# Kernel optimization log

Measured on AMD Instinct MI355X. Metric: run time of the kernel, lower is better.

Reference implementation:

```python
import jax, jax.numpy as jnp
import numpy as np

N = 100000       # nodes
E = 1600000      # edges (before self loops)
F_IN = 128       # input features
H = 4            # heads
C1, C2 = 32, 16  # per-head channels of conv1/conv2


def setup_inputs() -> dict:
    key = jax.random.key(0)
    ks = jax.random.split(key, 12)
    x = jax.random.normal(ks[0], (N, F_IN), jnp.float32)
    edge_index = jax.random.randint(ks[1], (2, E), 0, N, dtype=jnp.int32)
    s1 = 1.0 / np.sqrt(F_IN)
    s2 = 1.0 / np.sqrt(H * C1)
    return {
        "x": x,
        "edge_index": edge_index,
        "W1": jax.random.normal(ks[2], (F_IN, H * C1), jnp.float32) * s1,
        "a_src1": jax.random.normal(ks[3], (1, H, C1), jnp.float32) * s1,
        "a_dst1": jax.random.normal(ks[4], (1, H, C1), jnp.float32) * s1,
        "b1": jnp.zeros((H * C1,), jnp.float32),
        "W2": jax.random.normal(ks[5], (H * C1, H * C2), jnp.float32) * s2,
        "a_src2": jax.random.normal(ks[6], (1, H, C2), jnp.float32) * s2,
        "a_dst2": jax.random.normal(ks[7], (1, H, C2), jnp.float32) * s2,
        "b2": jnp.zeros((H * C2,), jnp.float32),
        "fc_w": jax.random.normal(ks[8], (H * C2, 2), jnp.float32) * (1.0 / np.sqrt(H * C2)),
        "fc_b": jnp.zeros((2,), jnp.float32),
    }


def gat_layer(x, edge_index, W, a_src, a_dst, b, heads, ch):
    """PyG GATConv: concat=True, negative_slope=0.2 (self loops already in edge_index)."""
    n = x.shape[0]
    h = (x @ W).reshape(n, heads, ch)                      # [N,H,C]
    alpha_src = jnp.sum(h * a_src, axis=-1)                # [N,H]
    alpha_dst = jnp.sum(h * a_dst, axis=-1)                # [N,H]
    src, dst = edge_index[0], edge_index[1]                # edge j->i: src=j, dst=i
    e = jax.nn.leaky_relu(alpha_src[src] + alpha_dst[dst], 0.2)  # [E,H]
    # scatter-softmax over incoming edges of each destination node
    m = jax.ops.segment_max(e, dst, num_segments=n)
    m = jnp.where(jnp.isfinite(m), m, 0.0)
    ex = jnp.exp(e - m[dst])
    s = jax.ops.segment_sum(ex, dst, num_segments=n)
    alpha = ex / s[dst]                                    # self loops guarantee s > 0
    out = jax.ops.segment_sum(alpha[:, :, None] * h[src], dst, num_segments=n)
    return out.reshape(n, heads * ch) + b


def reference(x, edge_index, W1, a_src1, a_dst1, b1, W2, a_src2, a_dst2, b2, fc_w, fc_b):
    n = x.shape[0]
    loops = jnp.arange(n, dtype=edge_index.dtype)
    ei = jnp.concatenate([edge_index, jnp.stack([loops, loops])], axis=1)  # add self loops once
    h = jax.nn.relu(gat_layer(x, ei, W1, a_src1, a_dst1, b1, H, C1))
    h = gat_layer(h, ei, W2, a_src2, a_dst2, b2, H, C2)
    g = jnp.sum(h, axis=0, keepdims=True)  # global_add_pool, batch = all zeros -> single graph
    return g @ fc_w + fc_b
```

## Files before the change

### kernel.cpp

```cpp
#include <hip/hip_runtime.h>
#include <hip/hip_bf16.h>
#include <math.h>


__device__ __forceinline__ float b2f(unsigned short u) {
    return __uint_as_float(((unsigned)u) << 16);
}
__device__ __forceinline__ unsigned short f2b(float f) {
    unsigned x = __float_as_uint(f);
    return (unsigned short)((x + 0x7fffu + ((x >> 16) & 1u)) >> 16);
}

struct alignas(16) us8 { unsigned short v[8]; };

typedef __attribute__((ext_vector_type(8))) short short8v;
typedef __attribute__((ext_vector_type(4))) float f32x4;


__global__ void init_k(int* __restrict__ bucketCnt, float* __restrict__ g) {
    int i = threadIdx.x;
    if (i < 512) bucketCnt[i] = 0;
    if (i < 66)  g[i] = 0.f;
}

__global__ void bucket_hist_k(const int* __restrict__ ei, int* __restrict__ bucketCnt,
                              int E, int N, int NB) {
    __shared__ int cnt[512];
    for (int t = threadIdx.x; t < 512; t += blockDim.x) cnt[t] = 0;
    __syncthreads();
    const int ITEMS = E + N;
    for (int i = blockIdx.x * blockDim.x + threadIdx.x; i < ITEMS;
         i += gridDim.x * blockDim.x) {
        int d = (i < E) ? ei[E + i] : (i - E);
        atomicAdd(&cnt[d >> 8], 1);
    }
    __syncthreads();
    for (int t = threadIdx.x; t < NB; t += blockDim.x)
        if (cnt[t]) atomicAdd(&bucketCnt[t], cnt[t]);
}

__global__ void bucket_scan_k(const int* __restrict__ bucketCnt,
                              int* __restrict__ bucketOff,
                              int* __restrict__ bucketFill, int NB) {
    __shared__ int ls[512];
    int t = threadIdx.x;
    int v = (t < NB) ? bucketCnt[t] : 0;
    ls[t] = v;
    __syncthreads();
    for (int off = 1; off < 512; off <<= 1) {
        int a = (t >= off) ? ls[t - off] : 0;
        __syncthreads();
        ls[t] += a;
        __syncthreads();
    }
    if (t < NB) { int e = ls[t] - v; bucketOff[t] = e; bucketFill[t] = e; }
}

__global__ __launch_bounds__(256) void bin_scatter_k(const int* __restrict__ ei,
                                                     int* __restrict__ bucketFill,
                                                     int2* __restrict__ binned,
                                                     int E, int N) {
    __shared__ int cnt[512];
    __shared__ int base[512];
    const int ITEMS = E + N;
    const int t = threadIdx.x;
    const int chunk0 = blockIdx.x * 4096;
    for (int b = t; b < 512; b += 256) cnt[b] = 0;
    __syncthreads();
    int s[16], d[16], r[16];
#pragma unroll
    for (int j = 0; j < 16; j++) {
        int i = chunk0 + j * 256 + t;
        if (i < ITEMS) {
            if (i < E) { s[j] = ei[i]; d[j] = ei[E + i]; }
            else       { s[j] = d[j] = i - E; }
            r[j] = atomicAdd(&cnt[d[j] >> 8], 1);
        } else d[j] = -1;
    }
    __syncthreads();
    for (int b = t; b < 512; b += 256) {
        int c = cnt[b];
        base[b] = c ? atomicAdd(&bucketFill[b], c) : 0;
    }
    __syncthreads();
#pragma unroll
    for (int j = 0; j < 16; j++)
        if (d[j] >= 0) binned[base[d[j] >> 8] + r[j]] = make_int2(s[j], d[j]);
}

__global__ void node_offs_k(const int2* __restrict__ binned,
                            const int* __restrict__ bucketOff,
                            const int* __restrict__ bucketCnt,
                            int* __restrict__ offs, int N, int ITEMS) {
    __shared__ int cnt[256];
    __shared__ int ls[256];
    const int b = blockIdx.x;
    const int t = threadIdx.x;
    cnt[t] = 0;
    __syncthreads();
    const int beg = bucketOff[b], c = bucketCnt[b];
    for (int i = t; i < c; i += 256)
        atomicAdd(&cnt[binned[beg + i].y & 255], 1);
    __syncthreads();
    int v = cnt[t];
    ls[t] = v;
    __syncthreads();
    for (int off = 1; off < 256; off <<= 1) {
        int a = (t >= off) ? ls[t - off] : 0;
        __syncthreads();
        ls[t] += a;
        __syncthreads();
    }
    int node = b * 256 + t;
    if (node < N) offs[node] = beg + ls[t] - v;
    if (node == N - 1) offs[N] = ITEMS;
}

__global__ void csr_scatter_k(const int2* __restrict__ binned,
                              const int* __restrict__ bucketOff,
                              const int* __restrict__ bucketCnt,
                              const int* __restrict__ offs, int* __restrict__ csr) {
    __shared__ int fill[256];
    const int b = blockIdx.x;
    fill[threadIdx.x] = 0;
    __syncthreads();
    const int beg = bucketOff[b], c = bucketCnt[b];
    for (int i = threadIdx.x; i < c; i += 256) {
        int2 sd = binned[beg + i];
        int r = atomicAdd(&fill[sd.y & 255], 1);
        csr[offs[sd.y] + r] = sd.x;
    }
}


template<int NCOL, bool XBF16>
__global__ __launch_bounds__(256) void gemm_alpha_mfma(
        const void* __restrict__ Xv, const float* __restrict__ W,
        const float* __restrict__ asrc, const float* __restrict__ adst,
        unsigned short* __restrict__ Y, float* __restrict__ As,
        float* __restrict__ Ad, int M) {
    constexpr int NT = NCOL / 16;
    __shared__ alignas(16) short alds[4 * 4 * 64 * 8];
    __shared__ alignas(16) short blds[NT * 4 * 64 * 8];

    const int t    = threadIdx.x;
    const int w    = t >> 6, lane = t & 63;
    const int row0 = blockIdx.x * 64;

    if constexpr (!XBF16) {
        const float* X = (const float*)Xv;
#pragma unroll
        for (int i = 0; i < 8; i++) {
            int flat = (i * 256 + t) * 4;
            int r = flat >> 7, k0 = flat & 127;
            int gr = row0 + r;
            float4 v = make_float4(0.f, 0.f, 0.f, 0.f);
            if (gr < M) v = *(const float4*)&X[(size_t)gr * 128 + k0];
            ushort4 u;
            u.x = f2b(v.x); u.y = f2b(v.y); u.z = f2b(v.z); u.w = f2b(v.w);
            int frag = ((r >> 4) * 4 + (k0 >> 5)) * 64 + ((((k0 & 31) >> 3) << 4) | (r & 15));
            *(ushort4*)&alds[frag * 8 + (k0 & 7)] = u;
        }
    } else {
        const unsigned short* X = (const unsigned short*)Xv;
#pragma unroll
        for (int i = 0; i < 4; i++) {
            int flat = (i * 256 + t) * 8;
            int r = flat >> 7, k0 = flat & 127;
            int gr = row0 + r;
            us8 v = {};
            if (gr < M) v = *(const us8*)&X[(size_t)gr * 128 + k0];
            int frag = ((r >> 4) * 4 + (k0 >> 5)) * 64 + ((((k0 & 31) >> 3) << 4) | (r & 15));
            *(us8*)&alds[frag * 8] = v;
        }
    }

    {
        constexpr int KQ = 256 / NCOL;
        constexpr int BITER = 32 / KQ;
        int c = t % NCOL, kq = t / NCOL;
        int nt = c >> 4, n = c & 15;
#pragma unroll
        for (int i = 0; i < BITER; i++) {
            int k0 = (i * KQ + kq) * 4;
            ushort4 u;
            u.x = f2b(W[(size_t)(k0 + 0) * NCOL + c]);
            u.y = f2b(W[(size_t)(k0 + 1) * NCOL + c]);
            u.z = f2b(W[(size_t)(k0 + 2) * NCOL + c]);
            u.w = f2b(W[(size_t)(k0 + 3) * NCOL + c]);
            int frag = (nt * 4 + (k0 >> 5)) * 64 + ((((k0 & 31) >> 3) << 4) | n);
            *(ushort4*)&blds[frag * 8 + (k0 & 7)] = u;
        }
    }
    __syncthreads();

    f32x4 acc[NT];
#pragma unroll
    for (int nt = 0; nt < NT; nt++) acc[nt] = (f32x4){0.f, 0.f, 0.f, 0.f};
#pragma unroll
    for (int ks = 0; ks < 4; ks++) {
        short8v a = *(short8v*)&alds[((w * 4 + ks) * 64 + lane) * 8];
#pragma unroll
        for (int nt = 0; nt < NT; nt++) {
            short8v b = *(short8v*)&blds[((nt * 4 + ks) * 64 + lane) * 8];
            acc[nt] = __builtin_amdgcn_mfma_f32_16x16x32_bf16(a, b, acc[nt], 0, 0, 0);
        }
    }

    const int g = lane >> 4, col = lane & 15;
    float ps[4][4] = {}, pd[4][4] = {};
#pragma unroll
    for (int nt = 0; nt < NT; nt++) {
        float av = asrc[nt * 16 + col];
        float dv = adst[nt * 16 + col];
        int h = (NCOL == 128) ? (nt >> 1) : nt;
#pragma unroll
        for (int j = 0; j < 4; j++) {
            float v = acc[nt][j];
            ps[j][h] = fmaf(v, av, ps[j][h]);
            pd[j][h] = fmaf(v, dv, pd[j][h]);
            int gr = row0 + w * 16 + 4 * g + j;
            if (gr < M) Y[(size_t)gr * NCOL + nt * 16 + col] = f2b(v);
        }
    }
#pragma unroll
    for (int m = 1; m < 16; m <<= 1) {
#pragma unroll
        for (int j = 0; j < 4; j++)
#pragma unroll
            for (int h = 0; h < 4; h++) {
                ps[j][h] += __shfl_xor(ps[j][h], m);
                pd[j][h] += __shfl_xor(pd[j][h], m);
            }
    }
    if (col == 0) {
#pragma unroll
        for (int j = 0; j < 4; j++) {
            int gr = row0 + w * 16 + 4 * g + j;
            if (gr < M) {
#pragma unroll
                for (int h = 0; h < 4; h++) {
                    As[gr * 4 + h] = ps[j][h];
                    Ad[gr * 4 + h] = pd[j][h];
                }
            }
        }
    }
}


template<bool RELU>
__global__ void agg128_k(const unsigned short* __restrict__ Hb,
                         const float* __restrict__ As, const float* __restrict__ Ad,
                         const int* __restrict__ offs, const int* __restrict__ csr,
                         const float* __restrict__ bias,
                         unsigned short* __restrict__ Outb, int n) {
    int wid  = (blockIdx.x * blockDim.x + threadIdx.x) >> 6;
    int lane = threadIdx.x & 63;
    if (wid >= n) return;
    const int g = lane >> 4;
    const int q = lane & 15;
    const int head = q >> 2;
    const int beg = offs[wid], end = offs[wid + 1];
    const float ad = Ad[wid * 4 + head];
    float acc[8];
#pragma unroll
    for (int k = 0; k < 8; k++) acc[k] = 0.f;
    float sw = 0.f;

    for (int cb = beg; cb < end; cb += 64) {
        const int nc = min(64, end - cb);
        const int sreg = csr[cb + (lane < nc ? lane : 0)];
        const int ncr = (nc + 7) & ~7;
        for (int j = 0; j < ncr; j += 8) {
            const int e0 = j + g, e1 = j + g + 4;
            const bool v0 = e0 < nc, v1 = e1 < nc;
            const int s0 = __shfl(sreg, v0 ? e0 : 0);
            const int s1 = __shfl(sreg, v1 ? e1 : 0);
            const us8 h0 = *(const us8*)&Hb[(size_t)s0 * 128 + q * 8];
            const us8 h1 = *(const us8*)&Hb[(size_t)s1 * 128 + q * 8];
            float ev0 = As[s0 * 4 + head] + ad; ev0 = ev0 > 0.f ? ev0 : 0.2f * ev0;
            float ev1 = As[s1 * 4 + head] + ad; ev1 = ev1 > 0.f ? ev1 : 0.2f * ev1;
            const float w0 = v0 ? __expf(ev0) : 0.f;
            const float w1 = v1 ? __expf(ev1) : 0.f;
            sw += w0 + w1;
#pragma unroll
            for (int k = 0; k < 8; k++) {
                acc[k] = fmaf(w0, b2f(h0.v[k]), acc[k]);
                acc[k] = fmaf(w1, b2f(h1.v[k]), acc[k]);
            }
        }
    }

    sw += __shfl_xor(sw, 16); sw += __shfl_xor(sw, 32);
#pragma unroll
    for (int k = 0; k < 8; k++) {
        acc[k] += __shfl_xor(acc[k], 16);
        acc[k] += __shfl_xor(acc[k], 32);
    }
    if (g == 0) {
        const float inv = 1.f / sw;
        us8 o;
#pragma unroll
        for (int k = 0; k < 8; k++) {
            float v = fmaf(acc[k], inv, bias[q * 8 + k]);
            if (RELU) v = fmaxf(v, 0.f);
            o.v[k] = f2b(v);
        }
        *(us8*)&Outb[(size_t)wid * 128 + q * 8] = o;
    }
}

__global__ void agg64_k(const unsigned short* __restrict__ Hb,
                        const float* __restrict__ As, const float* __restrict__ Ad,
                        const int* __restrict__ offs, const int* __restrict__ csr,
                        const float* __restrict__ bias,
                        float* __restrict__ Out, int n) {
    int wid  = (blockIdx.x * blockDim.x + threadIdx.x) >> 6;
    int lane = threadIdx.x & 63;
    if (wid >= n) return;
    const int g = lane >> 3;
    const int q = lane & 7;
    const int head = q >> 1;
    const int beg = offs[wid], end = offs[wid + 1];
    const float ad = Ad[wid * 4 + head];
    float acc[8];
#pragma unroll
    for (int k = 0; k < 8; k++) acc[k] = 0.f;
    float sw = 0.f;

    for (int cb = beg; cb < end; cb += 64) {
        const int nc = min(64, end - cb);
        const int sreg = csr[cb + (lane < nc ? lane : 0)];
        const int ncr = (nc + 15) & ~15;
        for (int j = 0; j < ncr; j += 16) {
            const int e0 = j + g, e1 = j + g + 8;
            const bool v0 = e0 < nc, v1 = e1 < nc;
            const int s0 = __shfl(sreg, v0 ? e0 : 0);
            const int s1 = __shfl(sreg, v1 ? e1 : 0);
            const us8 h0 = *(const us8*)&Hb[(size_t)s0 * 64 + q * 8];
            const us8 h1 = *(const us8*)&Hb[(size_t)s1 * 64 + q * 8];
            float ev0 = As[s0 * 4 + head] + ad; ev0 = ev0 > 0.f ? ev0 : 0.2f * ev0;
            float ev1 = As[s1 * 4 + head] + ad; ev1 = ev1 > 0.f ? ev1 : 0.2f * ev1;
            const float w0 = v0 ? __expf(ev0) : 0.f;
            const float w1 = v1 ? __expf(ev1) : 0.f;
            sw += w0 + w1;
#pragma unroll
            for (int k = 0; k < 8; k++) {
                acc[k] = fmaf(w0, b2f(h0.v[k]), acc[k]);
                acc[k] = fmaf(w1, b2f(h1.v[k]), acc[k]);
            }
        }
    }

    sw += __shfl_xor(sw, 8); sw += __shfl_xor(sw, 16); sw += __shfl_xor(sw, 32);
#pragma unroll
    for (int k = 0; k < 8; k++) {
        acc[k] += __shfl_xor(acc[k], 8);
        acc[k] += __shfl_xor(acc[k], 16);
        acc[k] += __shfl_xor(acc[k], 32);
    }
    if (g == 0) {
        const float inv = 1.f / sw;
        float4 o0, o1;
        o0.x = fmaf(acc[0], inv, bias[q * 8 + 0]);
        o0.y = fmaf(acc[1], inv, bias[q * 8 + 1]);
        o0.z = fmaf(acc[2], inv, bias[q * 8 + 2]);
        o0.w = fmaf(acc[3], inv, bias[q * 8 + 3]);
        o1.x = fmaf(acc[4], inv, bias[q * 8 + 4]);
        o1.y = fmaf(acc[5], inv, bias[q * 8 + 5]);
        o1.z = fmaf(acc[6], inv, bias[q * 8 + 6]);
        o1.w = fmaf(acc[7], inv, bias[q * 8 + 7]);
        *(float4*)&Out[(size_t)wid * 64 + q * 8]     = o0;
        *(float4*)&Out[(size_t)wid * 64 + q * 8 + 4] = o1;
    }
}


__global__ void pool_k(const float* __restrict__ h2, float* __restrict__ g, int n) {
    __shared__ float ls[256];
    int c   = threadIdx.x & 63;
    int rg  = (blockIdx.x * blockDim.x + threadIdx.x) >> 6;
    int nrg = (gridDim.x * blockDim.x) >> 6;
    float acc = 0.f;
    for (int r = rg; r < n; r += nrg) acc += h2[(size_t)r * 64 + c];
    ls[threadIdx.x] = acc;
    __syncthreads();
    if (threadIdx.x < 64) {
        float v = ls[threadIdx.x] + ls[threadIdx.x + 64] +
                  ls[threadIdx.x + 128] + ls[threadIdx.x + 192];
        atomicAdd(&g[c], v);
    }
}

__global__ void fc_k(const float* __restrict__ g, const float* __restrict__ w,
                     const float* __restrict__ b, float* __restrict__ out) {
    int j = threadIdx.x;
    if (j < 2) {
        float acc = b[j];
        for (int c = 0; c < 64; c++) acc = fmaf(g[c], w[c * 2 + j], acc);
        out[j] = acc;
    }
}


static inline size_t align256(size_t x) { return (x + 255) & ~(size_t)255; }

extern "C" void kernel_launch(void* const* d_in, const int* in_sizes, int n_in,
                              void* d_out, int out_size, void* d_ws, size_t ws_size,
                              hipStream_t stream) {
    const float* x     = (const float*)d_in[0];
    const int*   ei    = (const int*)  d_in[1];
    const float* W1    = (const float*)d_in[2];
    const float* asrc1 = (const float*)d_in[3];
    const float* adst1 = (const float*)d_in[4];
    const float* b1    = (const float*)d_in[5];
    const float* W2    = (const float*)d_in[6];
    const float* asrc2 = (const float*)d_in[7];
    const float* adst2 = (const float*)d_in[8];
    const float* b2    = (const float*)d_in[9];
    const float* fcw   = (const float*)d_in[10];
    const float* fcb   = (const float*)d_in[11];
    float* out = (float*)d_out;

    const int N = in_sizes[0] / 128;
    const int E = in_sizes[1] / 2;
    const int ITEMS = E + N;
    const int NB = (N + 255) >> 8;

    char* w = (char*)d_ws;
    size_t off = 0;
    int* offs  = (int*)(w + off); off = align256(off + (size_t)(N + 1) * 4);
    int* bCnt  = (int*)(w + off); off = align256(off + 512 * 4);
    int* bOff  = (int*)(w + off); off = align256(off + 512 * 4);
    int* bFill = (int*)(w + off); off = align256(off + 512 * 4);
    int* csr   = (int*)(w + off); off = align256(off + (size_t)ITEMS * 4);
    int2* binned = (int2*)(w + off); off = align256(off + (size_t)ITEMS * 8);
    float* As = (float*)(w + off); off = align256(off + (size_t)N * 4 * 4);
    float* Ad = (float*)(w + off); off = align256(off + (size_t)N * 4 * 4);
    float* g  = (float*)(w + off); off = align256(off + 66 * 4);
    unsigned short* bufH = (unsigned short*)(w + off); off = align256(off + (size_t)N * 128 * 2);
    unsigned short* bufO = (unsigned short*)(w + off); off = align256(off + (size_t)N * 128 * 4);
    float* out2 = (float*)bufO;

    init_k<<<1, 512, 0, stream>>>(bCnt, g);
    bucket_hist_k<<<1024, 256, 0, stream>>>(ei, bCnt, E, N, NB);
    bucket_scan_k<<<1, 512, 0, stream>>>(bCnt, bOff, bFill, NB);
    bin_scatter_k<<<(ITEMS + 4095) / 4096, 256, 0, stream>>>(ei, bFill, binned, E, N);
    node_offs_k<<<NB, 256, 0, stream>>>(binned, bOff, bCnt, offs, N, ITEMS);
    csr_scatter_k<<<NB, 256, 0, stream>>>(binned, bOff, bCnt, offs, csr);

    gemm_alpha_mfma<128, false><<<(N + 63) / 64, 256, 0, stream>>>(
        x, W1, asrc1, adst1, bufH, As, Ad, N);
    agg128_k<true><<<(N * 64 + 255) / 256, 256, 0, stream>>>(
        bufH, As, Ad, offs, csr, b1, bufO, N);

    gemm_alpha_mfma<64, true><<<(N + 63) / 64, 256, 0, stream>>>(
        bufO, W2, asrc2, adst2, bufH, As, Ad, N);
    agg64_k<<<(N * 64 + 255) / 256, 256, 0, stream>>>(
        bufH, As, Ad, offs, csr, b2, out2, N);

    pool_k<<<256, 256, 0, stream>>>(out2, g, N);
    fc_k<<<1, 64, 0, stream>>>(g, fcw, fcb, out);
}
```

Measured before the change: 279.4 us.

## Switch features to fp16, precompute per-edge weights once, use packed dot2 aggregation

Stores intermediate features and GEMM inputs as fp16 instead of bf16, using the f16 MFMA and packed conversion instructions. In the aggregation kernels, each lane now computes all four head attention weights for one edge once per 64-edge chunk. It stages them in LDS as fp16 instead of recomputing exp per lane per edge. The inner accumulation uses packed fp16 dot2 over two edges at once. This cuts the redundant exp/As gathers and the ALU work per edge, at the cost of fp16 range/precision risk (unnormalized exp weights in fp16 could overflow) and extra LDS traffic.

```diff
diff --git a/kernel.cpp b/kernel.cpp
--- a/kernel.cpp
+++ b/kernel.cpp
@@ -3,18 +3,27 @@
 #include <math.h>
 
 
-__device__ __forceinline__ float b2f(unsigned short u) {
-    return __uint_as_float(((unsigned)u) << 16);
-}
-__device__ __forceinline__ unsigned short f2b(float f) {
-    unsigned x = __float_as_uint(f);
-    return (unsigned short)((x + 0x7fffu + ((x >> 16) & 1u)) >> 16);
-}
-
-struct alignas(16) us8 { unsigned short v[8]; };
-
-typedef __attribute__((ext_vector_type(8))) short short8v;
+using pkh2 = decltype(__builtin_amdgcn_cvt_pkrtz(0.f, 0.f));
+typedef __fp16 half8v __attribute__((ext_vector_type(8)));
 typedef __attribute__((ext_vector_type(4))) float f32x4;
+
+__device__ __forceinline__ unsigned cvt2h(float a, float b) {
+    pkh2 r = __builtin_amdgcn_cvt_pkrtz(a, b);
+    return __builtin_bit_cast(unsigned, r);
+}
+__device__ __forceinline__ unsigned short f2h(float f) {
+    return __builtin_bit_cast(unsigned short, (_Float16)f);
+}
+
+__device__ __forceinline__ float fdot2b(unsigned wp, unsigned hp, float c) {
+#if __has_builtin(__builtin_amdgcn_fdot2)
+    return __builtin_amdgcn_fdot2(__builtin_bit_cast(pkh2, wp),
+                                  __builtin_bit_cast(pkh2, hp), c, false);
+#else
+    pkh2 w = __builtin_bit_cast(pkh2, wp), h = __builtin_bit_cast(pkh2, hp);
+    return fmaf((float)w[0], (float)h[0], fmaf((float)w[1], (float)h[1], c));
+#endif
+}
 
 
 __global__ void init_k(int* __restrict__ bucketCnt, float* __restrict__ g) {
@@ -133,7 +142,7 @@
 }
 
 
-template<int NCOL, bool XBF16>
+template<int NCOL, bool XF16>
 __global__ __launch_bounds__(256) void gemm_alpha_mfma(
         const void* __restrict__ Xv, const float* __restrict__ W,
         const float* __restrict__ asrc, const float* __restrict__ adst,
@@ -147,7 +156,7 @@
     const int w    = t >> 6, lane = t & 63;
     const int row0 = blockIdx.x * 64;
 
-    if constexpr (!XBF16) {
+    if constexpr (!XF16) {
         const float* X = (const float*)Xv;
 #pragma unroll
         for (int i = 0; i < 8; i++) {
@@ -156,10 +165,9 @@
             int gr = row0 + r;
             float4 v = make_float4(0.f, 0.f, 0.f, 0.f);
             if (gr < M) v = *(const float4*)&X[(size_t)gr * 128 + k0];
-            ushort4 u;
-            u.x = f2b(v.x); u.y = f2b(v.y); u.z = f2b(v.z); u.w = f2b(v.w);
+            uint2 u = make_uint2(cvt2h(v.x, v.y), cvt2h(v.z, v.w));
             int frag = ((r >> 4) * 4 + (k0 >> 5)) * 64 + ((((k0 & 31) >> 3) << 4) | (r & 15));
-            *(ushort4*)&alds[frag * 8 + (k0 & 7)] = u;
+            *(uint2*)&alds[frag * 8 + (k0 & 7)] = u;
         }
     } else {
         const unsigned short* X = (const unsigned short*)Xv;
@@ -168,10 +176,10 @@
             int flat = (i * 256 + t) * 8;
             int r = flat >> 7, k0 = flat & 127;
             int gr = row0 + r;
-            us8 v = {};
-            if (gr < M) v = *(const us8*)&X[(size_t)gr * 128 + k0];
+            uint4 v = make_uint4(0u, 0u, 0u, 0u);
+            if (gr < M) v = *(const uint4*)&X[(size_t)gr * 128 + k0];
             int frag = ((r >> 4) * 4 + (k0 >> 5)) * 64 + ((((k0 & 31) >> 3) << 4) | (r & 15));
-            *(us8*)&alds[frag * 8] = v;
+            *(uint4*)&alds[frag * 8] = v;
         }
     }
 
@@ -183,13 +191,11 @@
 #pragma unroll
         for (int i = 0; i < BITER; i++) {
             int k0 = (i * KQ + kq) * 4;
-            ushort4 u;
-            u.x = f2b(W[(size_t)(k0 + 0) * NCOL + c]);
-            u.y = f2b(W[(size_t)(k0 + 1) * NCOL + c]);
-            u.z = f2b(W[(size_t)(k0 + 2) * NCOL + c]);
-            u.w = f2b(W[(size_t)(k0 + 3) * NCOL + c]);
+            uint2 u = make_uint2(
+                cvt2h(W[(size_t)(k0 + 0) * NCOL + c], W[(size_t)(k0 + 1) * NCOL + c]),
+                cvt2h(W[(size_t)(k0 + 2) * NCOL + c], W[(size_t)(k0 + 3) * NCOL + c]));
             int frag = (nt * 4 + (k0 >> 5)) * 64 + ((((k0 & 31) >> 3) << 4) | n);
-            *(ushort4*)&blds[frag * 8 + (k0 & 7)] = u;
+            *(uint2*)&blds[frag * 8 + (k0 & 7)] = u;
         }
     }
     __syncthreads();
@@ -199,11 +205,11 @@
     for (int nt = 0; nt < NT; nt++) acc[nt] = (f32x4){0.f, 0.f, 0.f, 0.f};
 #pragma unroll
     for (int ks = 0; ks < 4; ks++) {
-        short8v a = *(short8v*)&alds[((w * 4 + ks) * 64 + lane) * 8];
+        half8v a = *(half8v*)&alds[((w * 4 + ks) * 64 + lane) * 8];
 #pragma unroll
         for (int nt = 0; nt < NT; nt++) {
-            short8v b = *(short8v*)&blds[((nt * 4 + ks) * 64 + lane) * 8];
-            acc[nt] = __builtin_amdgcn_mfma_f32_16x16x32_bf16(a, b, acc[nt], 0, 0, 0);
+            half8v b = *(half8v*)&blds[((nt * 4 + ks) * 64 + lane) * 8];
+            acc[nt] = __builtin_amdgcn_mfma_f32_16x16x32_f16(a, b, acc[nt], 0, 0, 0);
         }
     }
 
@@ -220,7 +226,7 @@
             ps[j][h] = fmaf(v, av, ps[j][h]);
             pd[j][h] = fmaf(v, dv, pd[j][h]);
             int gr = row0 + w * 16 + 4 * g + j;
-            if (gr < M) Y[(size_t)gr * NCOL + nt * 16 + col] = f2b(v);
+            if (gr < M) Y[(size_t)gr * NCOL + nt * 16 + col] = f2h(v);
         }
     }
 #pragma unroll
@@ -255,59 +261,84 @@
                          const int* __restrict__ offs, const int* __restrict__ csr,
                          const float* __restrict__ bias,
                          unsigned short* __restrict__ Outb, int n) {
+    __shared__ unsigned short wlds[4][4 * 64];
     int wid  = (blockIdx.x * blockDim.x + threadIdx.x) >> 6;
     int lane = threadIdx.x & 63;
     if (wid >= n) return;
+    const int wv = (threadIdx.x >> 6) & 3;
     const int g = lane >> 4;
     const int q = lane & 15;
     const int head = q >> 2;
     const int beg = offs[wid], end = offs[wid + 1];
-    const float ad = Ad[wid * 4 + head];
+    const float4 ad4 = *(const float4*)&Ad[wid * 4];
     float acc[8];
 #pragma unroll
     for (int k = 0; k < 8; k++) acc[k] = 0.f;
-    float sw = 0.f;
+    float4 sw4 = make_float4(0.f, 0.f, 0.f, 0.f);
 
     for (int cb = beg; cb < end; cb += 64) {
         const int nc = min(64, end - cb);
-        const int sreg = csr[cb + (lane < nc ? lane : 0)];
+        const int sreg = csr[cb + min(lane, nc - 1)];
+        {
+            const float4 as4 = *(const float4*)&As[(size_t)sreg * 4];
+            float w0 = 0.f, w1 = 0.f, w2 = 0.f, w3 = 0.f;
+            if (lane < nc) {
+                float e0 = as4.x + ad4.x; e0 = e0 > 0.f ? e0 : 0.2f * e0;
+                float e1 = as4.y + ad4.y; e1 = e1 > 0.f ? e1 : 0.2f * e1;
+                float e2 = as4.z + ad4.z; e2 = e2 > 0.f ? e2 : 0.2f * e2;
+                float e3 = as4.w + ad4.w; e3 = e3 > 0.f ? e3 : 0.2f * e3;
+                w0 = __expf(e0); w1 = __expf(e1); w2 = __expf(e2); w3 = __expf(e3);
+            }
+            sw4.x += w0; sw4.y += w1; sw4.z += w2; sw4.w += w3;
+            wlds[wv][0 * 64 + lane] = f2h(w0);
+            wlds[wv][1 * 64 + lane] = f2h(w1);
+            wlds[wv][2 * 64 + lane] = f2h(w2);
+            wlds[wv][3 * 64 + lane] = f2h(w3);
+        }
+        asm volatile("" ::: "memory");
         const int ncr = (nc + 7) & ~7;
         for (int j = 0; j < ncr; j += 8) {
-            const int e0 = j + g, e1 = j + g + 4;
-            const bool v0 = e0 < nc, v1 = e1 < nc;
-            const int s0 = __shfl(sreg, v0 ? e0 : 0);
-            const int s1 = __shfl(sreg, v1 ? e1 : 0);
-            const us8 h0 = *(const us8*)&Hb[(size_t)s0 * 128 + q * 8];
-            const us8 h1 = *(const us8*)&Hb[(size_t)s1 * 128 + q * 8];
-            float ev0 = As[s0 * 4 + head] + ad; ev0 = ev0 > 0.f ? ev0 : 0.2f * ev0;
-            float ev1 = As[s1 * 4 + head] + ad; ev1 = ev1 > 0.f ? ev1 : 0.2f * ev1;
-            const float w0 = v0 ? __expf(ev0) : 0.f;
-            const float w1 = v1 ? __expf(ev1) : 0.f;
-            sw += w0 + w1;
-#pragma unroll
-            for (int k = 0; k < 8; k++) {
-                acc[k] = fmaf(w0, b2f(h0.v[k]), acc[k]);
-                acc[k] = fmaf(w1, b2f(h1.v[k]), acc[k]);
+            const int e0 = j + 2 * g;
+            const int s0 = __shfl(sreg, e0);
+            const int s1 = __shfl(sreg, e0 + 1);
+            const unsigned wlo = wlds[wv][head * 64 + e0];
+            const unsigned whi = wlds[wv][head * 64 + e0 + 1];
+            const unsigned wp = wlo | (whi << 16);
+            const uint4 h0 = *(const uint4*)&Hb[(size_t)s0 * 128 + q * 8];
+            const uint4 h1 = *(const uint4*)&Hb[(size_t)s1 * 128 + q * 8];
+#pragma unroll
+            for (int k = 0; k < 4; k++) {
+                unsigned d0 = (&h0.x)[k], d1 = (&h1.x)[k];
+                acc[2 * k]     = fdot2b(wp, __builtin_amdgcn_perm(d1, d0, 0x05040100u), acc[2 * k]);
+                acc[2 * k + 1] = fdot2b(wp, __builtin_amdgcn_perm(d1, d0, 0x07060302u), acc[2 * k + 1]);
             }
         }
     }
 
-    sw += __shfl_xor(sw, 16); sw += __shfl_xor(sw, 32);
+#pragma unroll
+    for (int m = 1; m < 64; m <<= 1) {
+        sw4.x += __shfl_xor(sw4.x, m); sw4.y += __shfl_xor(sw4.y, m);
+        sw4.z += __shfl_xor(sw4.z, m); sw4.w += __shfl_xor(sw4.w, m);
+    }
 #pragma unroll
     for (int k = 0; k < 8; k++) {
         acc[k] += __shfl_xor(acc[k], 16);
         acc[k] += __shfl_xor(acc[k], 32);
     }
     if (g == 0) {
-        const float inv = 1.f / sw;
-        us8 o;
+        float swh = head < 2 ? (head == 0 ? sw4.x : sw4.y)
+                             : (head == 2 ? sw4.z : sw4.w);
+        const float inv = 1.f / swh;
+        float o[8];
 #pragma unroll
         for (int k = 0; k < 8; k++) {
             float v = fmaf(acc[k], inv, bias[q * 8 + k]);
             if (RELU) v = fmaxf(v, 0.f);
-            o.v[k] = f2b(v);
-        }
-        *(us8*)&Outb[(size_t)wid * 128 + q * 8] = o;
+            o[k] = v;
+        }
+        uint4 ov = make_uint4(cvt2h(o[0], o[1]), cvt2h(o[2], o[3]),
+                              cvt2h(o[4], o[5]), cvt2h(o[6], o[7]));
+        *(uint4*)&Outb[(size_t)wid * 128 + q * 8] = ov;
     }
 }
 
@@ -316,44 +347,65 @@
                         const int* __restrict__ offs, const int* __restrict__ csr,
                         const float* __restrict__ bias,
                         float* __restrict__ Out, int n) {
+    __shared__ unsigned short wlds[4][4 * 64];
     int wid  = (blockIdx.x * blockDim.x + threadIdx.x) >> 6;
     int lane = threadIdx.x & 63;
     if (wid >= n) return;
+    const int wv = (threadIdx.x >> 6) & 3;
     const int g = lane >> 3;
     const int q = lane & 7;
     const int head = q >> 1;
     const int beg = offs[wid], end = offs[wid + 1];
-    const float ad = Ad[wid * 4 + head];
+    const float4 ad4 = *(const float4*)&Ad[wid * 4];
     float acc[8];
 #pragma unroll
     for (int k = 0; k < 8; k++) acc[k] = 0.f;
-    float sw = 0.f;
+    float4 sw4 = make_float4(0.f, 0.f, 0.f, 0.f);
 
     for (int cb = beg; cb < end; cb += 64) {
         const int nc = min(64, end - cb);
-        const int sreg = csr[cb + (lane < nc ? lane : 0)];
+        const int sreg = csr[cb + min(lane, nc - 1)];
+        {
+            const float4 as4 = *(const float4*)&As[(size_t)sreg * 4];
+            float w0 = 0.f, w1 = 0.f, w2 = 0.f, w3 = 0.f;
+            if (lane < nc) {
+                float e0 = as4.x + ad4.x; e0 = e0 > 0.f ? e0 : 0.2f * e0;
+                float e1 = as4.y + ad4.y; e1 = e1 > 0.f ? e1 : 0.2f * e1;
+                float e2 = as4.z + ad4.z; e2 = e2 > 0.f ? e2 : 0.2f * e2;
+                float e3 = as4.w + ad4.w; e3 = e3 > 0.f ? e3 : 0.2f * e3;
+                w0 = __expf(e0); w1 = __expf(e1); w2 = __expf(e2); w3 = __expf(e3);
+            }
+            sw4.x += w0; sw4.y += w1; sw4.z += w2; sw4.w += w3;
+            wlds[wv][0 * 64 + lane] = f2h(w0);
+            wlds[wv][1 * 64 + lane] = f2h(w1);
+            wlds[wv][2 * 64 + lane] = f2h(w2);
+            wlds[wv][3 * 64 + lane] = f2h(w3);
+        }
+        asm volatile("" ::: "memory");
         const int ncr = (nc + 15) & ~15;
         for (int j = 0; j < ncr; j += 16) {
-            const int e0 = j + g, e1 = j + g + 8;
-            const bool v0 = e0 < nc, v1 = e1 < nc;
-            const int s0 = __shfl(sreg, v0 ? e0 : 0);
-            const int s1 = __shfl(sreg, v1 ? e1 : 0);
-            const us8 h0 = *(const us8*)&Hb[(size_t)s0 * 64 + q * 8];
-            const us8 h1 = *(const us8*)&Hb[(size_t)s1 * 64 + q * 8];
-            float ev0 = As[s0 * 4 + head] + ad; ev0 = ev0 > 0.f ? ev0 : 0.2f * ev0;
-            float ev1 = As[s1 * 4 + head] + ad; ev1 = ev1 > 0.f ? ev1 : 0.2f * ev1;
-            const float w0 = v0 ? __expf(ev0) : 0.f;
-            const float w1 = v1 ? __expf(ev1) : 0.f;
-            sw += w0 + w1;
-#pragma unroll
-            for (int k = 0; k < 8; k++) {
-                acc[k] = fmaf(w0, b2f(h0.v[k]), acc[k]);
-                acc[k] = fmaf(w1, b2f(h1.v[k]), acc[k]);
+            const int e0 = j + 2 * g;
+            const int s0 = __shfl(sreg, e0);
+            const int s1 = __shfl(sreg, e0 + 1);
+            const unsigned wlo = wlds[wv][head * 64 + e0];
+            const unsigned whi = wlds[wv][head * 64 + e0 + 1];
+            const unsigned wp = wlo | (whi << 16);
+            const uint4 h0 = *(const uint4*)&Hb[(size_t)s0 * 64 + q * 8];
+            const uint4 h1 = *(const uint4*)&Hb[(size_t)s1 * 64 + q * 8];
+#pragma unroll
+            for (int k = 0; k < 4; k++) {
+                unsigned d0 = (&h0.x)[k], d1 = (&h1.x)[k];
+                acc[2 * k]     = fdot2b(wp, __builtin_amdgcn_perm(d1, d0, 0x05040100u), acc[2 * k]);
+                acc[2 * k + 1] = fdot2b(wp, __builtin_amdgcn_perm(d1, d0, 0x07060302u), acc[2 * k + 1]);
             }
         }
     }
 
-    sw += __shfl_xor(sw, 8); sw += __shfl_xor(sw, 16); sw += __shfl_xor(sw, 32);
+#pragma unroll
+    for (int m = 1; m < 64; m <<= 1) {
+        sw4.x += __shfl_xor(sw4.x, m); sw4.y += __shfl_xor(sw4.y, m);
+        sw4.z += __shfl_xor(sw4.z, m); sw4.w += __shfl_xor(sw4.w, m);
+    }
 #pragma unroll
     for (int k = 0; k < 8; k++) {
         acc[k] += __shfl_xor(acc[k], 8);
@@ -361,7 +413,9 @@
         acc[k] += __shfl_xor(acc[k], 32);
     }
     if (g == 0) {
-        const float inv = 1.f / sw;
+        float swh = head < 2 ? (head == 0 ? sw4.x : sw4.y)
+                             : (head == 2 ? sw4.z : sw4.w);
+        const float inv = 1.f / swh;
         float4 o0, o1;
         o0.x = fmaf(acc[0], inv, bias[q * 8 + 0]);
         o0.y = fmaf(acc[1], inv, bias[q * 8 + 1]);
```

Measured after the change: 294.4 us. 5.4% more time.
